# Kernel tuning notes

Measured on AMD Instinct MI355X. Metric: run time of the kernel, lower is better.

## Reference

```python
import jax, jax.numpy as jnp
import numpy as np

NODE_NUM = 2000
D_MODEL = 2048
IN_DIM = 7
OUT_DIM = 1
NODE_DIM = 40
CONV_CH = 64
SKIP_CH = 64
DEPTH = 3
ALPHA = 0.05
BATCH = 64
KERNEL = D_MODEL - NODE_NUM + 1  # 49
LN_EPS = 1e-5


def setup_inputs() -> dict:
    key = jax.random.key(0)
    ks = jax.random.split(key, 12)
    s = 0.02
    return {
        "x": jax.random.normal(ks[0], (BATCH, IN_DIM * D_MODEL), dtype=jnp.float32),
        "nodevec1": jax.random.normal(ks[1], (NODE_NUM, NODE_DIM), dtype=jnp.float32),
        "nodevec2": jax.random.normal(ks[2], (NODE_DIM, NODE_NUM), dtype=jnp.float32),
        "w_start": jax.random.normal(ks[3], (CONV_CH, IN_DIM, KERNEL), dtype=jnp.float32) * s,
        "b_start": jnp.zeros((CONV_CH,), dtype=jnp.float32),
        "w_mlp": jax.random.normal(ks[4], (SKIP_CH, (DEPTH + 1) * CONV_CH), dtype=jnp.float32) * s,
        "b_mlp": jnp.zeros((SKIP_CH,), dtype=jnp.float32),
        "w_end": jax.random.normal(ks[5], (OUT_DIM, SKIP_CH), dtype=jnp.float32) * s,
        "b_end": jnp.zeros((OUT_DIM,), dtype=jnp.float32),
        "w_lin": jax.random.normal(ks[6], (D_MODEL, NODE_NUM), dtype=jnp.float32) * s,
        "b_lin": jnp.zeros((D_MODEL,), dtype=jnp.float32),
        "ln_g": jnp.ones((D_MODEL,), dtype=jnp.float32),
        "ln_b": jnp.zeros((D_MODEL,), dtype=jnp.float32),
    }


def _conv1d(x, w, b):
    # x: (B, Cin, L), w: (Cout, Cin, K) -> (B, Cout, L-K+1)
    y = jax.lax.conv_general_dilated(x, w, window_strides=(1,), padding='VALID',
                                     dimension_numbers=('NCH', 'OIH', 'NCH'))
    return y + b[None, :, None]


def _layernorm(x, g, b):
    mu = jnp.mean(x, axis=-1, keepdims=True)
    var = jnp.mean(jnp.square(x - mu), axis=-1, keepdims=True)
    return (x - mu) * jax.lax.rsqrt(var + LN_EPS) * g + b


def reference(x, nodevec1, nodevec2, w_start, b_start, w_mlp, b_mlp,
              w_end, b_end, w_lin, b_lin, ln_g, ln_b):
    # adaptive adjacency: softmax(relu(E1 @ E2), axis=1)
    adp = jax.nn.softmax(jax.nn.relu(nodevec1 @ nodevec2), axis=1)  # (N, N)

    out = x.reshape(x.shape[0], IN_DIM, D_MODEL)
    out = _conv1d(out, w_start, b_start)  # (B, CONV_CH, N)

    # mixprop
    adj = adp + jnp.eye(NODE_NUM, dtype=adp.dtype)
    a = adj / jnp.sum(adj, axis=1, keepdims=True)  # row-normalized (N, N)
    h = out
    hops = [h]
    for _ in range(DEPTH):
        # einsum('ncw,vw->ncv', h, a)
        h = ALPHA * out + (1.0 - ALPHA) * jnp.einsum('bcw,vw->bcv', h, a)
        hops.append(h)
    ho = jnp.concatenate(hops, axis=1)  # (B, (DEPTH+1)*CONV_CH, N)
    ho = jnp.einsum('bcn,oc->bon', ho, w_mlp) + b_mlp[None, :, None]  # 1x1 conv

    out = jax.nn.gelu(ho, approximate=False)
    out = jnp.einsum('bcn,oc->bon', out, w_end) + b_end[None, :, None]  # (B, 1, N)
    out = jnp.squeeze(out, axis=1)  # (B, N)
    out = out @ w_lin.T + b_lin  # (B, D_MODEL)
    out = _layernorm(out, ln_g, ln_b)
    return out.reshape(out.shape[0], -1)
```

## Files before the change

kernel.cpp:

```cpp
#include <hip/hip_runtime.h>

#define NODE_NUM 2000
#define DM 2048
#define IN_DIM 7
#define CONV_CH 64
#define KER 49
#define BATCH 64

typedef __attribute__((ext_vector_type(8))) short bf16x8;
typedef __attribute__((ext_vector_type(4))) float f32x4;
typedef __attribute__((ext_vector_type(4))) unsigned int u32x4;

__device__ __forceinline__ float bf2f(unsigned short u) {
  union { unsigned int i; float f; } c; c.i = ((unsigned int)u) << 16; return c.f;
}
__device__ __forceinline__ unsigned short f2bf(float f) {
  union { float f; unsigned int i; } c; c.f = f;
  unsigned int r = c.i + 0x7FFFu + ((c.i >> 16) & 1u);
  return (unsigned short)(r >> 16);
}

__global__ __launch_bounds__(256) void adj_kernel(const float* __restrict__ nv1,
                                                  const float* __restrict__ nv2,
                                                  unsigned short* __restrict__ Ab) {
  const int bid = blockIdx.x;
  const int tid = threadIdx.x;
  if (bid >= 500) {
    const int r0 = 2000 + (bid - 500) * 4;
    for (int i = tid; i < 4 * 2048; i += 256)
      Ab[(size_t)(r0 + (i >> 11)) * DM + (i & 2047)] = 0;
    return;
  }
  const int v0 = bid * 4;
  __shared__ float e1s[4][40];
  __shared__ float redm[4][4], redsum[4][4];
  for (int i = tid; i < 160; i += 256) e1s[i / 40][i % 40] = nv1[(v0 + i / 40) * 40 + i % 40];
  __syncthreads();
  const int w0 = tid * 8;
  const bool oob = (w0 >= NODE_NUM);
  const float* base = nv2 + (oob ? 0 : w0);
  float acc[4][8] = {};
  f32x4 xa = *(const f32x4*)(base);
  f32x4 xb = *(const f32x4*)(base + 4);
  for (int k = 0; k < 40; ++k) {
    const f32x4 ca = xa, cb = xb;
    if (k < 39) {
      xa = *(const f32x4*)(base + (k + 1) * NODE_NUM);
      xb = *(const f32x4*)(base + (k + 1) * NODE_NUM + 4);
    }
#pragma unroll
    for (int v = 0; v < 4; ++v) {
      const float e = e1s[v][k];
#pragma unroll
      for (int i = 0; i < 4; ++i) {
        acc[v][i]     = fmaf(e, ca[i], acc[v][i]);
        acc[v][i + 4] = fmaf(e, cb[i], acc[v][i + 4]);
      }
    }
  }
  const int wid = tid >> 6, lane = tid & 63;
#pragma unroll
  for (int v = 0; v < 4; ++v) {
    float mx = -1e30f;
    if (!oob) {
#pragma unroll
      for (int i = 0; i < 8; ++i) {
        acc[v][i] = fmaxf(acc[v][i], 0.f);
        mx = fmaxf(mx, acc[v][i]);
      }
    }
    for (int o = 32; o; o >>= 1) mx = fmaxf(mx, __shfl_xor(mx, o));
    if (lane == 0) redm[v][wid] = mx;
  }
  __syncthreads();
#pragma unroll
  for (int v = 0; v < 4; ++v) {
    const float mx = fmaxf(fmaxf(redm[v][0], redm[v][1]), fmaxf(redm[v][2], redm[v][3]));
    float sum = 0.f;
    if (!oob) {
#pragma unroll
      for (int i = 0; i < 8; ++i) { const float e = __expf(acc[v][i] - mx); acc[v][i] = e; sum += e; }
    }
    for (int o = 32; o; o >>= 1) sum += __shfl_xor(sum, o);
    if (lane == 0) redsum[v][wid] = sum;
  }
  __syncthreads();
#pragma unroll
  for (int v = 0; v < 4; ++v) {
    const float sum = redsum[v][0] + redsum[v][1] + redsum[v][2] + redsum[v][3];
    const float inv = 0.5f / sum;
    const int vg = v0 + v;
    unsigned short out[8];
#pragma unroll
    for (int i = 0; i < 8; ++i) {
      const float val = oob ? 0.f : (acc[v][i] * inv + ((w0 + i == vg) ? 0.5f : 0.f));
      out[i] = f2bf(val);
    }
    *(u32x4*)(Ab + (size_t)vg * DM + w0) = *(const u32x4*)out;
  }
}

__global__ __launch_bounds__(256) void wpack_kernel(const float* __restrict__ wst,
                                                    unsigned short* __restrict__ wpack) {
  const int idx = blockIdx.x * 256 + threadIdx.x;
  const int e = idx & 7;
  const int lane = (idx >> 3) & 63;
  const int w = (idx >> 9) & 3;
  const int kstep = idx >> 11;
  const int c = w * 16 + (lane & 15);
  const int k = kstep * 32 + (lane >> 4) * 8 + e;
  const int ci = k >> 6, kern = k & 63;
  const float val = (kern < KER) ? wst[(c * IN_DIM + ci) * KER + kern] : 0.f;
  wpack[idx] = f2bf(val);
}

__global__ __launch_bounds__(256) void wmpack_kernel(const float* __restrict__ wm,
                                                     unsigned short* __restrict__ wmb) {
  const int idx = blockIdx.x * 256 + threadIdx.x;
  wmb[idx] = f2bf(wm[idx]);
}

__global__ __launch_bounds__(256) void conv_kernel(const float* __restrict__ x,
                                                   const unsigned short* __restrict__ wpack,
                                                   const float* __restrict__ bst,
                                                   unsigned short* __restrict__ H0) {
  __shared__ alignas(16) unsigned short xcopy[8 * 7 * 128];
  const int b = blockIdx.y;
  const int n0 = blockIdx.x * 64;
  const int tid = threadIdx.x;
  const int wv = tid >> 6, lane = tid & 63;
  const int l15 = lane & 15, kg = lane >> 4;
  bf16x8 af[14];
#pragma unroll
  for (int ks = 0; ks < 14; ++ks)
    af[ks] = *(const bf16x8*)(wpack + ((size_t)(ks * 4 + wv) * 64 + lane) * 8);
  f32x4 acc[4];
  {
    const f32x4 bv = *(const f32x4*)(bst + wv * 16 + kg * 4);
#pragma unroll
    for (int nf = 0; nf < 4; ++nf) acc[nf] = bv;
  }
  const size_t xb = (size_t)b * (IN_DIM * DM);
#pragma unroll
  for (int it = 0; it < 14; ++it) {
    const int row = it * 4 + (tid >> 6);
    const int s = row / 7, ci = row % 7;
    const int j = (tid & 63) * 2;
    int g0 = n0 + j + s;     if (g0 > DM - 1) g0 = DM - 1;
    int g1 = n0 + j + 1 + s; if (g1 > DM - 1) g1 = DM - 1;
    const float v0 = x[xb + ci * DM + g0];
    const float v1 = x[xb + ci * DM + g1];
    const unsigned int pk = (unsigned int)f2bf(v0) | ((unsigned int)f2bf(v1) << 16);
    *(unsigned int*)((char*)xcopy + row * 256 + j * 2) = pk;
  }
  __syncthreads();
#pragma unroll
  for (int ks = 0; ks < 14; ++ks) {
    const int ci = ks >> 1;
    const int kern0 = ((ks & 1) << 5) + kg * 8;
#pragma unroll
    for (int nf = 0; nf < 4; ++nf) {
      const int q = nf * 16 + l15 + kern0;
      const int byte = ((q & 7) * 7 + ci) * 256 + (q & ~7) * 2;
      const bf16x8 bfr = *(const bf16x8*)((const char*)xcopy + byte);
      acc[nf] = __builtin_amdgcn_mfma_f32_16x16x32_bf16(af[ks], bfr, acc[nf], 0, 0, 0);
    }
  }
#pragma unroll
  for (int nf = 0; nf < 4; ++nf) {
#pragma unroll
    for (int r = 0; r < 4; ++r) {
      const int c = wv * 16 + kg * 4 + r;
      const int n = n0 + nf * 16 + l15;
      H0[(size_t)(b * 64 + c) * DM + n] =
          (n < NODE_NUM) ? f2bf(acc[nf][r]) : (unsigned short)0;
    }
  }
}

template <int MODE>
__global__ __launch_bounds__(256) void gemm_nt(const unsigned short* __restrict__ A,
                                               const unsigned short* __restrict__ Bt,
                                               const unsigned short* __restrict__ H0,
                                               void* __restrict__ Cout) {
  __shared__ alignas(16) unsigned short As[2][128 * 64];
  __shared__ alignas(16) unsigned short Bs[2][128 * 64];
  const int tid = threadIdx.x;
  int bx, by;
  if (MODE == 0) {
    const int lin = blockIdx.y * 16 + blockIdx.x;
    const int swz = (lin & 7) * 64 + (lin >> 3);
    bx = swz & 15;  by = swz >> 4;
  } else {
    bx = blockIdx.x;  by = blockIdx.y;
  }
  const int n0 = bx * 128;
  const int m0 = (MODE == 0) ? by * 128 : 0;
  const int kbeg = (MODE == 0) ? 0 : by * 256;
  const int nt = (MODE == 0) ? (DM / 64) : 4;
  const int wid = tid >> 6, lane = tid & 63;
  const int wr = wid >> 1, wc = wid & 1;
  const int l15 = lane & 15, kg = lane >> 4;

  auto STAGE = [&](int buf, int k0) {
#pragma unroll
    for (int it = 0; it < 4; ++it) {
      const int lin = it * 4096 + tid * 16;
      const int row = lin >> 7;
      const int blog = (lin & 127) ^ ((row & 7) << 4);
      const char* sa = (const char*)A + ((size_t)(m0 + row) * DM + k0) * 2 + blog;
      const char* sb = (const char*)Bt + ((size_t)(n0 + row) * DM + k0) * 2 + blog;
      __builtin_amdgcn_global_load_lds((const __attribute__((address_space(1))) void*)sa,
                                       (__attribute__((address_space(3))) void*)((char*)As[buf] + lin),
                                       16, 0, 0);
      __builtin_amdgcn_global_load_lds((const __attribute__((address_space(1))) void*)sb,
                                       (__attribute__((address_space(3))) void*)((char*)Bs[buf] + lin),
                                       16, 0, 0);
    }
  };

  f32x4 acc[4][4] = {};
  STAGE(0, kbeg);
  STAGE(1, kbeg + 64);

  for (int t = 0; t < nt; ++t) {
    const int cur = t & 1;
    if (t + 1 < nt) asm volatile("s_waitcnt vmcnt(8)" ::: "memory");
    else            asm volatile("s_waitcnt vmcnt(0)" ::: "memory");
    __builtin_amdgcn_s_barrier();
    __builtin_amdgcn_sched_barrier(0);
    bf16x8 af[2][4], bfr[2][4];
#pragma unroll
    for (int f = 0; f < 4; ++f) {
      const int ra = wr * 64 + f * 16 + l15;
      const int rb = wc * 64 + f * 16 + l15;
#pragma unroll
      for (int kk = 0; kk < 2; ++kk) {
        const int off = kk * 64 + kg * 16;
        af[kk][f]  = *(const bf16x8*)((const char*)As[cur] + ra * 128 + (off ^ ((ra & 7) << 4)));
        bfr[kk][f] = *(const bf16x8*)((const char*)Bs[cur] + rb * 128 + (off ^ ((rb & 7) << 4)));
      }
    }
#pragma unroll
    for (int kk = 0; kk < 2; ++kk)
#pragma unroll
      for (int mf = 0; mf < 4; ++mf)
#pragma unroll
        for (int nf = 0; nf < 4; ++nf)
          acc[mf][nf] = __builtin_amdgcn_mfma_f32_16x16x32_bf16(af[kk][mf], bfr[kk][nf],
                                                                acc[mf][nf], 0, 0, 0);
    __syncthreads();
    if (t + 2 < nt) STAGE(cur, kbeg + (t + 2) * 64);
  }
  const int l4 = lane >> 4;
#pragma unroll
  for (int mf = 0; mf < 4; ++mf) {
#pragma unroll
    for (int nf = 0; nf < 4; ++nf) {
#pragma unroll
      for (int r = 0; r < 4; ++r) {
        const int gm = m0 + wr * 64 + mf * 16 + l4 * 4 + r;
        const int gn = n0 + wc * 64 + nf * 16 + l15;
        if (MODE == 0) {
          const float v = 0.05f * bf2f(H0[(size_t)gm * DM + gn]) + 0.95f * acc[mf][nf][r];
          ((unsigned short*)Cout)[(size_t)gm * DM + gn] = f2bf(v);
        } else {
          if (gm < 64)
            ((float*)Cout)[(size_t)blockIdx.y * 64 * DM + (size_t)gm * DM + gn] = acc[mf][nf][r];
        }
      }
    }
  }
}

__global__ __launch_bounds__(256) void mlp_kernel(const unsigned short* __restrict__ h0,
                                                  const unsigned short* __restrict__ h1,
                                                  const unsigned short* __restrict__ h2,
                                                  const unsigned short* __restrict__ h3,
                                                  const unsigned short* __restrict__ wmb,
                                                  const float* __restrict__ bm,
                                                  const float* __restrict__ we,
                                                  const float* __restrict__ be,
                                                  unsigned short* __restrict__ out1) {
  __shared__ alignas(16) unsigned short hs[64 * 264];
  __shared__ alignas(16) unsigned short wl[64 * 264];
  __shared__ float cbuf[128];
  const int b = blockIdx.y;
  const int gn0 = blockIdx.x * 64;
  const int tid = threadIdx.x;
#pragma unroll
  for (int it = 0; it < 8; ++it) {
    const int idx = it * 256 + tid;
    const int o = idx >> 5, c = (idx & 31) * 8;
    *(bf16x8*)&wl[o * 264 + c] = *(const bf16x8*)(wmb + o * 256 + c);
  }
  if (tid < 64) cbuf[tid] = bm[tid];
  else if (tid < 128) cbuf[tid] = we[tid - 64];
  char* hsb = (char*)hs;
#pragma unroll
  for (int it = 0; it < 8; ++it) {
    const int idx = it * 256 + tid;
    const int cf = idx >> 3, n0 = (idx & 7) * 8;
    const int hop = cf >> 6, c = cf & 63;
    const unsigned short* hb = (hop == 0) ? h0 : (hop == 1) ? h1 : (hop == 2) ? h2 : h3;
    const unsigned long long* p =
        (const unsigned long long*)(hb + (size_t)(b * 64 + c) * DM + gn0 + n0);
    const unsigned long long lo = p[0], hi = p[1];
#pragma unroll
    for (int t = 0; t < 8; ++t) {
      const int i = (t + tid) & 7;
      const unsigned short val = (unsigned short)(((i & 4) ? hi : lo) >> ((i & 3) * 16));
      *(unsigned short*)(hsb + (n0 + i) * 528 + cf * 2) = val;
    }
  }
  __syncthreads();
  const int wid = tid >> 6, lane = tid & 63;
  const int l15 = lane & 15, kg = lane >> 4;
  const char* wb = (const char*)wl;
  f32x4 acc[4] = {};
#pragma unroll
  for (int kk = 0; kk < 8; ++kk) {
    const int koff = kk * 64 + kg * 16;
    const bf16x8 bfr = *(const bf16x8*)(hsb + (wid * 16 + l15) * 528 + koff);
#pragma unroll
    for (int mf = 0; mf < 4; ++mf) {
      const bf16x8 af = *(const bf16x8*)(wb + (mf * 16 + l15) * 528 + koff);
      acc[mf] = __builtin_amdgcn_mfma_f32_16x16x32_bf16(af, bfr, acc[mf], 0, 0, 0);
    }
  }
  float pl = 0.f;
#pragma unroll
  for (int mf = 0; mf < 4; ++mf) {
#pragma unroll
    for (int r = 0; r < 4; ++r) {
      const int o = mf * 16 + kg * 4 + r;
      const float s = acc[mf][r] + cbuf[o];
      const float g = 0.5f * s * (1.f + erff(s * 0.70710678118f));
      pl += cbuf[64 + o] * g;
    }
  }
  pl += __shfl_xor(pl, 16);
  pl += __shfl_xor(pl, 32);
  if (kg == 0) {
    const int n = gn0 + wid * 16 + l15;
    out1[(size_t)b * DM + n] = (n < NODE_NUM) ? f2bf(pl + be[0]) : (unsigned short)0;
  }
}

__global__ __launch_bounds__(256) void wlin_cvt(const float* __restrict__ wlin,
                                                unsigned short* __restrict__ wl) {
  const int idx = (blockIdx.x * 256 + threadIdx.x) * 8;
  const int d = idx >> 11, w0 = idx & 2047;
  unsigned short out[8];
#pragma unroll
  for (int j = 0; j < 8; ++j) {
    const int w = w0 + j;
    out[j] = (w < NODE_NUM) ? f2bf(wlin[d * NODE_NUM + w]) : (unsigned short)0;
  }
  *(u32x4*)(wl + idx) = *(const u32x4*)out;
}

__global__ __launch_bounds__(256) void ln_kernel(const float* __restrict__ yp,
                                                 const float* __restrict__ bl,
                                                 const float* __restrict__ g,
                                                 const float* __restrict__ bb,
                                                 float* __restrict__ out) {
  const int b = blockIdx.x, tid = threadIdx.x;
  __shared__ float rs[4], rq[4];
  float v[8];
  float s = 0.f;
#pragma unroll
  for (int i = 0; i < 8; ++i) {
    const int d = i * 256 + tid;
    float acc = bl[d];
#pragma unroll
    for (int sp = 0; sp < 8; ++sp) acc += yp[(size_t)sp * 64 * DM + (size_t)b * DM + d];
    v[i] = acc;
    s += acc;
  }
  for (int o = 32; o; o >>= 1) s += __shfl_xor(s, o);
  const int wid = tid >> 6, lane = tid & 63;
  if (lane == 0) rs[wid] = s;
  __syncthreads();
  s = rs[0] + rs[1] + rs[2] + rs[3];
  const float mu = s * (1.f / 2048.f);
  float q = 0.f;
#pragma unroll
  for (int i = 0; i < 8; ++i) { const float d = v[i] - mu; q += d * d; }
  for (int o = 32; o; o >>= 1) q += __shfl_xor(q, o);
  if (lane == 0) rq[wid] = q;
  __syncthreads();
  q = rq[0] + rq[1] + rq[2] + rq[3];
  const float inv = rsqrtf(q * (1.f / 2048.f) + 1e-5f);
#pragma unroll
  for (int i = 0; i < 8; ++i) {
    const int d = i * 256 + tid;
    out[(size_t)b * DM + d] = (v[i] - mu) * inv * g[d] + bb[d];
  }
}

extern "C" void kernel_launch(void* const* d_in, const int* in_sizes, int n_in,
                              void* d_out, int out_size, void* d_ws, size_t ws_size,
                              hipStream_t stream) {
  const float* x      = (const float*)d_in[0];
  const float* nv1    = (const float*)d_in[1];
  const float* nv2    = (const float*)d_in[2];
  const float* w_st   = (const float*)d_in[3];
  const float* b_st   = (const float*)d_in[4];
  const float* w_mlp  = (const float*)d_in[5];
  const float* b_mlp  = (const float*)d_in[6];
  const float* w_end  = (const float*)d_in[7];
  const float* b_end  = (const float*)d_in[8];
  const float* w_lin  = (const float*)d_in[9];
  const float* b_lin  = (const float*)d_in[10];
  const float* ln_g   = (const float*)d_in[11];
  const float* ln_b   = (const float*)d_in[12];

  char* ws = (char*)d_ws;
  const size_t SZ_A = (size_t)DM * DM * 2;
  const size_t SZ_H = (size_t)4096 * DM * 2;
  unsigned short* Ab    = (unsigned short*)(ws);
  unsigned short* H0    = (unsigned short*)(ws + SZ_A);
  unsigned short* H1    = (unsigned short*)(ws + SZ_A + SZ_H);
  unsigned short* H2    = (unsigned short*)(ws + SZ_A + 2 * SZ_H);
  unsigned short* H3    = (unsigned short*)(ws + SZ_A + 3 * SZ_H);
  unsigned short* OUT1  = (unsigned short*)(ws + SZ_A + 4 * SZ_H);
  unsigned short* WPACK = (unsigned short*)(ws + SZ_A + 4 * SZ_H + 262144);
  unsigned short* WMB   = (unsigned short*)(ws + SZ_A + 4 * SZ_H + 319488);
  unsigned short* WL    = (unsigned short*)(ws + SZ_A + 4 * SZ_H + 524288);
  float*          YP    = (float*)(ws + SZ_A + 4 * SZ_H + 524288 + SZ_A);

  wpack_kernel<<<112, 256, 0, stream>>>(w_st, WPACK);
  wmpack_kernel<<<64, 256, 0, stream>>>(w_mlp, WMB);
  adj_kernel<<<512, 256, 0, stream>>>(nv1, nv2, Ab);
  conv_kernel<<<dim3(32, BATCH), 256, 0, stream>>>(x, WPACK, b_st, H0);
  wlin_cvt<<<2048, 256, 0, stream>>>(w_lin, WL);

  gemm_nt<0><<<dim3(16, 32), 256, 0, stream>>>(H0, Ab, H0, (void*)H1);
  gemm_nt<0><<<dim3(16, 32), 256, 0, stream>>>(H1, Ab, H0, (void*)H2);
  gemm_nt<0><<<dim3(16, 32), 256, 0, stream>>>(H2, Ab, H0, (void*)H3);

  mlp_kernel<<<dim3(32, BATCH), 256, 0, stream>>>(H0, H1, H2, H3, WMB, b_mlp,
                                                  w_end, b_end, OUT1);
  gemm_nt<1><<<dim3(16, 8), 256, 0, stream>>>(OUT1, WL, (const unsigned short*)0, (void*)YP);
  ln_kernel<<<BATCH, 256, 0, stream>>>(YP, b_lin, ln_g, ln_b, (float*)d_out);
}
```

Baseline: 271.2 us.

## Load A operand directly to registers in mixprop GEMM, stage only B in LDS

Splits the templated GEMM into a dedicated mixprop kernel and a tail kernel. The mixprop kernel reads its A fragments straight from global memory into registers instead of staging them through LDS, halving LDS use (32KB instead of 64KB). It also changes the pipeline to single-prefetch of B with one barrier per iteration. This is meant to cut LDS traffic and raise occupancy, but each wave now issues uncoalesced-ish 16-byte global loads for A and the B prefetch depth is shallower, so latency may be exposed.

```diff
diff --git a/kernel.cpp b/kernel.cpp
--- a/kernel.cpp
+++ b/kernel.cpp
@@ -178,26 +178,96 @@
   }
 }
 
-template <int MODE>
-__global__ __launch_bounds__(256) void gemm_nt(const unsigned short* __restrict__ A,
+__global__ __launch_bounds__(256) void gemm_ad(const unsigned short* __restrict__ A,
                                                const unsigned short* __restrict__ Bt,
                                                const unsigned short* __restrict__ H0,
-                                               void* __restrict__ Cout) {
+                                               unsigned short* __restrict__ C) {
+  __shared__ alignas(16) unsigned short Bs[2][128 * 64];
+  const int tid = threadIdx.x;
+  const int lin = blockIdx.y * 16 + blockIdx.x;
+  const int swz = (lin & 7) * 64 + (lin >> 3);
+  const int bx = swz & 15, by = swz >> 4;
+  const int n0 = bx * 128, m0 = by * 128;
+  const int wid = tid >> 6, lane = tid & 63;
+  const int wr = wid >> 1, wc = wid & 1;
+  const int l15 = lane & 15, kg = lane >> 4;
+
+  auto STAGE_B = [&](int buf, int k0) {
+#pragma unroll
+    for (int it = 0; it < 4; ++it) {
+      const int linb = it * 4096 + tid * 16;
+      const int row = linb >> 7;
+      const int blog = (linb & 127) ^ ((row & 7) << 4);
+      const char* sb = (const char*)Bt + ((size_t)(n0 + row) * DM + k0) * 2 + blog;
+      __builtin_amdgcn_global_load_lds((const __attribute__((address_space(1))) void*)sb,
+                                       (__attribute__((address_space(3))) void*)((char*)Bs[buf] + linb),
+                                       16, 0, 0);
+    }
+  };
+
+  const unsigned short* aptr = A + (size_t)(m0 + wr * 64 + l15) * DM + kg * 8;
+
+  f32x4 acc[4][4] = {};
+  STAGE_B(0, 0);
+
+  for (int t = 0; t < 32; ++t) {
+    const int cur = t & 1;
+    const int k0 = t * 64;
+    bf16x8 af[2][4];
+#pragma unroll
+    for (int f = 0; f < 4; ++f)
+#pragma unroll
+      for (int kk = 0; kk < 2; ++kk)
+        af[kk][f] = *(const bf16x8*)(aptr + (size_t)f * 16 * DM + kk * 32 + k0);
+    asm volatile("s_waitcnt vmcnt(8)" ::: "memory");
+    __builtin_amdgcn_s_barrier();
+    __builtin_amdgcn_sched_barrier(0);
+    bf16x8 bfr[2][4];
+#pragma unroll
+    for (int f = 0; f < 4; ++f) {
+      const int rb = wc * 64 + f * 16 + l15;
+#pragma unroll
+      for (int kk = 0; kk < 2; ++kk) {
+        const int off = kk * 64 + kg * 16;
+        bfr[kk][f] = *(const bf16x8*)((const char*)Bs[cur] + rb * 128 + (off ^ ((rb & 7) << 4)));
+      }
+    }
+    if (t + 1 < 32) STAGE_B(cur ^ 1, k0 + 64);
+#pragma unroll
+    for (int kk = 0; kk < 2; ++kk)
+#pragma unroll
+      for (int mf = 0; mf < 4; ++mf)
+#pragma unroll
+        for (int nf = 0; nf < 4; ++nf)
+          acc[mf][nf] = __builtin_amdgcn_mfma_f32_16x16x32_bf16(af[kk][mf], bfr[kk][nf],
+                                                                acc[mf][nf], 0, 0, 0);
+  }
+  const int l4 = lane >> 4;
+#pragma unroll
+  for (int mf = 0; mf < 4; ++mf) {
+#pragma unroll
+    for (int nf = 0; nf < 4; ++nf) {
+#pragma unroll
+      for (int r = 0; r < 4; ++r) {
+        const int gm = m0 + wr * 64 + mf * 16 + l4 * 4 + r;
+        const int gn = n0 + wc * 64 + nf * 16 + l15;
+        const float v = 0.05f * bf2f(H0[(size_t)gm * DM + gn]) + 0.95f * acc[mf][nf][r];
+        C[(size_t)gm * DM + gn] = f2bf(v);
+      }
+    }
+  }
+}
+
+__global__ __launch_bounds__(256) void gemm_tail(const unsigned short* __restrict__ A,
+                                                 const unsigned short* __restrict__ Bt,
+                                                 float* __restrict__ Cout) {
   __shared__ alignas(16) unsigned short As[2][128 * 64];
   __shared__ alignas(16) unsigned short Bs[2][128 * 64];
   const int tid = threadIdx.x;
-  int bx, by;
-  if (MODE == 0) {
-    const int lin = blockIdx.y * 16 + blockIdx.x;
-    const int swz = (lin & 7) * 64 + (lin >> 3);
-    bx = swz & 15;  by = swz >> 4;
-  } else {
-    bx = blockIdx.x;  by = blockIdx.y;
-  }
+  const int bx = blockIdx.x, by = blockIdx.y;
   const int n0 = bx * 128;
-  const int m0 = (MODE == 0) ? by * 128 : 0;
-  const int kbeg = (MODE == 0) ? 0 : by * 256;
-  const int nt = (MODE == 0) ? (DM / 64) : 4;
+  const int kbeg = by * 256;
+  const int nt = 4;
   const int wid = tid >> 6, lane = tid & 63;
   const int wr = wid >> 1, wc = wid & 1;
   const int l15 = lane & 15, kg = lane >> 4;
@@ -208,7 +278,7 @@
       const int lin = it * 4096 + tid * 16;
       const int row = lin >> 7;
       const int blog = (lin & 127) ^ ((row & 7) << 4);
-      const char* sa = (const char*)A + ((size_t)(m0 + row) * DM + k0) * 2 + blog;
+      const char* sa = (const char*)A + ((size_t)row * DM + k0) * 2 + blog;
       const char* sb = (const char*)Bt + ((size_t)(n0 + row) * DM + k0) * 2 + blog;
       __builtin_amdgcn_global_load_lds((const __attribute__((address_space(1))) void*)sa,
                                        (__attribute__((address_space(3))) void*)((char*)As[buf] + lin),
@@ -259,15 +329,10 @@
     for (int nf = 0; nf < 4; ++nf) {
 #pragma unroll
       for (int r = 0; r < 4; ++r) {
-        const int gm = m0 + wr * 64 + mf * 16 + l4 * 4 + r;
+        const int gm = wr * 64 + mf * 16 + l4 * 4 + r;
         const int gn = n0 + wc * 64 + nf * 16 + l15;
-        if (MODE == 0) {
-          const float v = 0.05f * bf2f(H0[(size_t)gm * DM + gn]) + 0.95f * acc[mf][nf][r];
-          ((unsigned short*)Cout)[(size_t)gm * DM + gn] = f2bf(v);
-        } else {
-          if (gm < 64)
-            ((float*)Cout)[(size_t)blockIdx.y * 64 * DM + (size_t)gm * DM + gn] = acc[mf][nf][r];
-        }
+        if (gm < 64)
+          Cout[(size_t)by * 64 * DM + (size_t)gm * DM + gn] = acc[mf][nf][r];
       }
     }
   }
@@ -436,12 +501,12 @@
   conv_kernel<<<dim3(32, BATCH), 256, 0, stream>>>(x, WPACK, b_st, H0);
   wlin_cvt<<<2048, 256, 0, stream>>>(w_lin, WL);
 
-  gemm_nt<0><<<dim3(16, 32), 256, 0, stream>>>(H0, Ab, H0, (void*)H1);
-  gemm_nt<0><<<dim3(16, 32), 256, 0, stream>>>(H1, Ab, H0, (void*)H2);
-  gemm_nt<0><<<dim3(16, 32), 256, 0, stream>>>(H2, Ab, H0, (void*)H3);
+  gemm_ad<<<dim3(16, 32), 256, 0, stream>>>(H0, Ab, H0, H1);
+  gemm_ad<<<dim3(16, 32), 256, 0, stream>>>(H1, Ab, H0, H2);
+  gemm_ad<<<dim3(16, 32), 256, 0, stream>>>(H2, Ab, H0, H3);
 
   mlp_kernel<<<dim3(32, BATCH), 256, 0, stream>>>(H0, H1, H2, H3, WMB, b_mlp,
                                                   w_end, b_end, OUT1);
-  gemm_nt<1><<<dim3(16, 8), 256, 0, stream>>>(OUT1, WL, (const unsigned short*)0, (void*)YP);
+  gemm_tail<<<dim3(16, 8), 256, 0, stream>>>(OUT1, WL, YP);
   ln_kernel<<<BATCH, 256, 0, stream>>>(YP, b_lin, ln_g, ln_b, (float*)d_out);
 }
```

Result: slower. 372.9 us (+37.5%).
